# Kernel tuning notes

Measured on AMD Instinct MI355X. Metric: run time of the kernel, lower is better.

Reference implementation:

```python
import jax, jax.numpy as jnp
import numpy as np

N_NODES = 100000
N_EDGES = 1600000
D_IN = 64
D_OUT = 64


def setup_inputs() -> dict:
    key = jax.random.key(0)
    k1, k2, k3, k4, k5 = jax.random.split(key, 5)
    feat = jax.random.normal(k1, (N_NODES, D_IN), dtype=jnp.float32)
    src = jax.random.randint(k2, (N_EDGES,), 0, N_NODES, dtype=jnp.int64)
    dst = jax.random.randint(k3, (N_EDGES,), 0, N_NODES, dtype=jnp.int64)
    # Xavier-uniform init with relu gain, as in reset_parameters()
    gain = np.sqrt(2.0)
    bound = gain * np.sqrt(6.0 / (D_IN + D_OUT))
    W_self = jax.random.uniform(k4, (D_OUT, D_IN), minval=-bound, maxval=bound, dtype=jnp.float32)
    W_neigh = jax.random.uniform(k5, (D_OUT, D_IN), minval=-bound, maxval=bound, dtype=jnp.float32)
    return {"feat": feat, "src": src, "dst": dst, "W_self": W_self, "W_neigh": W_neigh}


def _spmm_mean(feat, src, dst, n_nodes):
    # Mean neighbor aggregation: for each dst node, average src features.
    gathered = feat[src]  # [E, D] irregular gather
    agg = jax.ops.segment_sum(gathered, dst, num_segments=n_nodes)  # [N, D]
    deg = jax.ops.segment_sum(jnp.ones((src.shape[0],), feat.dtype), dst, num_segments=n_nodes)
    return agg / jnp.maximum(deg, 1.0)[:, None]


def reference(feat, src, dst, W_self, W_neigh):
    neigh = _spmm_mean(feat, src, dst, feat.shape[0])  # [N, D_in]
    # rst = fc_self(feat) + fc_neigh(SpMM(feat))
    return feat @ W_self.T + neigh @ W_neigh.T
```

## Files before the change

kernel.cpp:

```cpp
#include <hip/hip_runtime.h>
#include <hip/hip_fp16.h>

#define N_NODES 100000
#define N_EDGES 1600000
#define D 64
#define ZROW 100000

#define NPB   240
#define NB    417
#define CAP   8192

#define EPB   8192
#define PBLK  ((N_EDGES + EPB - 1) / EPB)
#define CONVB 256

#define W3_FF16     0u
#define W3_PACKED   12800128u
#define W3_GCUR     (W3_PACKED + 4u * NB * CAP)
#define W3_NODEOFF  (W3_GCUR + 4u * NB)
#define W3_NODECNT  (W3_NODEOFF + 4u * N_NODES)
#define W3_W16      (W3_NODECNT + 4u * N_NODES)
#define W3_NEED     (W3_W16 + 16384u)

typedef __attribute__((ext_vector_type(8))) _Float16 half8;
typedef __attribute__((ext_vector_type(4))) float f32x4;

__device__ inline unsigned int h2bits(__half2 h) { return *(unsigned int*)&h; }
__device__ inline __half2 bits2h(unsigned int u) { return *(__half2*)&u; }
__device__ inline __half2 h2shfl_xor(__half2 x, int mask) {
    int i = *(int*)&x;
    i = __shfl_xor(i, mask);
    return *(__half2*)&i;
}

__global__ __launch_bounds__(1024) void k_part_conv(
    const float* __restrict__ feat,
    const int* __restrict__ src, const int* __restrict__ dst,
    const float* __restrict__ Ws, const float* __restrict__ Wn,
    unsigned int* __restrict__ ff16, unsigned int* __restrict__ w16,
    int* __restrict__ gcur, int* __restrict__ packed)
{
    __shared__ int recs[EPB];
    __shared__ int cnt[NB];
    __shared__ int scn[512];
    __shared__ int pos[NB];
    __shared__ int cur[NB];
    __shared__ int dlt[NB];

    const int bid = blockIdx.x;
    const int t   = threadIdx.x;

    if (bid >= PBLK) {
        if (bid < PBLK + CONVB) {
            const int total = N_NODES * D / 8;
            for (int i = (bid - PBLK) * 1024 + t; i < total; i += CONVB * 1024) {
                const float4 x = ((const float4*)feat)[i * 2];
                const float4 y = ((const float4*)feat)[i * 2 + 1];
                uint4 o;
                o.x = h2bits(__floats2half2_rn(x.x, x.y));
                o.y = h2bits(__floats2half2_rn(x.z, x.w));
                o.z = h2bits(__floats2half2_rn(y.x, y.y));
                o.w = h2bits(__floats2half2_rn(y.z, y.w));
                ((uint4*)ff16)[i] = o;
            }
        } else {
            for (int i = t; i < 2048; i += 1024) {
                w16[i]        = h2bits(__floats2half2_rn(Ws[2 * i], Ws[2 * i + 1]));
                w16[2048 + i] = h2bits(__floats2half2_rn(Wn[2 * i], Wn[2 * i + 1]));
            }
            if (t < 32) ff16[ZROW * 32 + t] = 0;
        }
        return;
    }

    const int e0 = bid * EPB;
    const int nE = min(EPB, N_EDGES - e0);

    for (int i = t; i < NB; i += 1024) cnt[i] = 0;
    __syncthreads();

    int pk[8], bk[8];
    #pragma unroll
    for (int k = 0; k < 8; ++k) {
        const int i = t + k * 1024;
        if (i < nE) {
            const int d  = dst[e0 + i];
            const int b  = d / NPB;
            const int dl = d - b * NPB;
            pk[k] = src[e0 + i] | (dl << 17);
            bk[k] = b;
            atomicAdd(&cnt[b], 1);
        } else {
            bk[k] = -1;
        }
    }
    __syncthreads();

    if (t < 512) scn[t] = (t < NB) ? cnt[t] : 0;
    __syncthreads();
    for (int o = 1; o < 512; o <<= 1) {
        int x = 0;
        if (t < 512 && t >= o) x = scn[t - o];
        __syncthreads();
        if (t < 512) scn[t] += x;
        __syncthreads();
    }
    if (t < NB) {
        const int v    = cnt[t];
        const int excl = scn[t] - v;
        pos[t] = excl;
        cur[t] = excl;
        dlt[t] = atomicAdd(&gcur[t], v);
    }
    __syncthreads();

    #pragma unroll
    for (int k = 0; k < 8; ++k) {
        if (bk[k] >= 0) {
            const int p = atomicAdd(&cur[bk[k]], 1);
            recs[p] = pk[k];
        }
    }
    __syncthreads();

    const int w    = t >> 6;
    const int lane = t & 63;
    for (int b = w; b < NB; b += 16) {
        const int n = cnt[b];
        const int o = pos[b];
        const int g = b * CAP + dlt[b];
        for (int i = lane; i < n; i += 64)
            packed[g + i] = recs[o + i];
    }
}

__global__ __launch_bounds__(512) void k_sortb(
    const int* __restrict__ gcur,
    int* packed,
    int* __restrict__ node_off, int* __restrict__ node_cnt)
{
    __shared__ int recs[CAP];
    __shared__ int lcnt[256];
    __shared__ int sc[256];
    __shared__ int lcur[NPB];

    const int t      = threadIdx.x;
    const int bucket = blockIdx.x;
    const int base   = bucket * CAP;
    int total = gcur[bucket];
    if (total > CAP) total = CAP;

    if (t < 256) lcnt[t] = 0;
    __syncthreads();

    for (int i = t; i < total; i += 512) {
        const int r = packed[base + i];
        recs[i] = r;
        atomicAdd(&lcnt[r >> 17], 1);
    }
    __syncthreads();

    if (t < 256) sc[t] = lcnt[t];
    __syncthreads();
    for (int o = 1; o < 256; o <<= 1) {
        int x = 0;
        if (t < 256 && t >= o) x = sc[t - o];
        __syncthreads();
        if (t < 256) sc[t] += x;
        __syncthreads();
    }

    if (t < NPB) {
        const int excl = sc[t] - lcnt[t];
        lcur[t] = excl;
        const int n = bucket * NPB + t;
        if (n < N_NODES) {
            node_off[n] = base + excl;
            node_cnt[n] = lcnt[t];
        }
    }
    __syncthreads();

    for (int i = t; i < total; i += 512) {
        const int r   = recs[i];
        const int pos = atomicAdd(&lcur[r >> 17], 1);
        packed[base + pos] = r & 0x1FFFF;
    }
}

__global__ __launch_bounds__(256) void k_agg_f16(
    const unsigned int* __restrict__ ff16,
    const int* __restrict__ node_off,
    const int* __restrict__ node_cnt,
    const int* __restrict__ packed,
    float* __restrict__ out)
{
    const int gtid = blockIdx.x * 256 + threadIdx.x;
    const int n    = gtid >> 6;
    const int lane = gtid & 63;
    if (n >= N_NODES) return;

    const int start = node_off[n];
    const int deg   = node_cnt[n];
    const int sub   = lane >> 3;
    const int chunk = lane & 7;

    __half2 a0 = __floats2half2_rn(0.f, 0.f);
    __half2 a1 = a0, a2 = a0, a3 = a0;

    for (int b = 0; b < deg; b += 64) {
        const int rem = min(deg - b, 64);
        int p = ZROW;
        if (lane < rem) p = packed[start + b + lane];

        const int npair = (rem + 15) >> 4;
        for (int q = 0; q < npair; ++q) {
            const int e0 = q * 16 + sub;
            const int s0 = __shfl(p, e0)     & 0x1FFFF;
            const int s1 = __shfl(p, e0 + 8) & 0x1FFFF;
            const uint4 v0 = ((const uint4*)ff16)[(size_t)s0 * 8 + chunk];
            const uint4 v1 = ((const uint4*)ff16)[(size_t)s1 * 8 + chunk];
            a0 += bits2h(v0.x);
            a1 += bits2h(v0.y);
            a2 += bits2h(v0.z);
            a3 += bits2h(v0.w);
            a0 += bits2h(v1.x);
            a1 += bits2h(v1.y);
            a2 += bits2h(v1.z);
            a3 += bits2h(v1.w);
        }
    }

    #pragma unroll
    for (int mask = 8; mask <= 32; mask <<= 1) {
        a0 += h2shfl_xor(a0, mask);
        a1 += h2shfl_xor(a1, mask);
        a2 += h2shfl_xor(a2, mask);
        a3 += h2shfl_xor(a3, mask);
    }

    if (lane < 8) {
        const float inv = 1.0f / (float)((deg > 0) ? deg : 1);
        uint4 mb;
        mb.x = h2bits(__floats2half2_rn(__low2float(a0) * inv, __high2float(a0) * inv));
        mb.y = h2bits(__floats2half2_rn(__low2float(a1) * inv, __high2float(a1) * inv));
        mb.z = h2bits(__floats2half2_rn(__low2float(a2) * inv, __high2float(a2) * inv));
        mb.w = h2bits(__floats2half2_rn(__low2float(a3) * inv, __high2float(a3) * inv));
        ((uint4*)out)[(size_t)n * 16 + lane] = mb;
    }
}

__global__ __launch_bounds__(256) void k_update_mfma(
    const unsigned int* __restrict__ ff16,
    const _Float16* __restrict__ w16,
    float* out)
{
    const int wv   = threadIdx.x >> 6;
    const int lane = threadIdx.x & 63;
    const int n0   = blockIdx.x * 64 + wv * 16;
    const int r16  = lane & 15;
    const int g    = lane >> 4;

    half8 bws[4][2], bwn[4][2];
    #pragma unroll
    for (int nt = 0; nt < 4; ++nt) {
        const int c = nt * 16 + r16;
        #pragma unroll
        for (int kt = 0; kt < 2; ++kt) {
            const int k0 = kt * 32 + g * 8;
            bws[nt][kt] = *(const half8*)(w16 + c * 64 + k0);
            bwn[nt][kt] = *(const half8*)(w16 + 4096 + c * 64 + k0);
        }
    }

    const int arow = n0 + r16;
    const int rc   = (arow < N_NODES) ? arow : (N_NODES - 1);

    f32x4 acc[4] = {{0.f,0.f,0.f,0.f}, {0.f,0.f,0.f,0.f},
                    {0.f,0.f,0.f,0.f}, {0.f,0.f,0.f,0.f}};

    #pragma unroll
    for (int kt = 0; kt < 2; ++kt) {
        const int k8 = kt * 4 + g;
        const uint4 af_u = ((const uint4*)ff16)[(size_t)rc * 8 + k8];
        const uint4 am_u = ((const uint4*)out )[(size_t)rc * 16 + k8];
        const half8 af = *(const half8*)&af_u;
        const half8 am = *(const half8*)&am_u;
        #pragma unroll
        for (int nt = 0; nt < 4; ++nt) {
            acc[nt] = __builtin_amdgcn_mfma_f32_16x16x32_f16(af, bws[nt][kt], acc[nt], 0, 0, 0);
            acc[nt] = __builtin_amdgcn_mfma_f32_16x16x32_f16(am, bwn[nt][kt], acc[nt], 0, 0, 0);
        }
    }

    #pragma unroll
    for (int nt = 0; nt < 4; ++nt) {
        #pragma unroll
        for (int r = 0; r < 4; ++r) {
            const int ro = n0 + g * 4 + r;
            if (ro < N_NODES)
                out[(size_t)ro * 64 + nt * 16 + r16] = acc[nt][r];
        }
    }
}

__global__ __launch_bounds__(256) void sage_scatter(
    const float* __restrict__ feat,
    const int*   __restrict__ src,
    const int*   __restrict__ dst,
    float*       __restrict__ agg,
    float*       __restrict__ deg)
{
    const int gtid = blockIdx.x * blockDim.x + threadIdx.x;
    const int edge = gtid >> 6;
    const int lane = gtid & 63;
    if (edge >= N_EDGES) return;
    const int s = src[edge];
    const int d = dst[edge];
    atomicAdd(&agg[d * D + lane], feat[s * D + lane]);
    if (lane == 0) atomicAdd(&deg[d], 1.0f);
}

#define RL(v, l) __int_as_float(__builtin_amdgcn_readlane(__float_as_int(v), (l)))

__global__ __launch_bounds__(256) void k_update_div(
    const float* __restrict__ feat,
    const float* __restrict__ Ws,
    const float* __restrict__ Wn,
    const float* __restrict__ deg,
    float* out)
{
    const int wid   = (blockIdx.x * 256 + threadIdx.x) >> 6;
    const int lane  = threadIdx.x & 63;
    const int nwave = (gridDim.x * 256) >> 6;

    const float4* Ws4 = (const float4*)Ws;
    const float4* Wn4 = (const float4*)Wn;
    float4 ws[16], wn[16];
    #pragma unroll
    for (int j = 0; j < 16; ++j) {
        ws[j] = Ws4[lane * 16 + j];
        wn[j] = Wn4[lane * 16 + j];
    }

    for (int n = wid; n < N_NODES; n += nwave) {
        const float f = feat[n * D + lane];
        const float a = out[n * D + lane] / fmaxf(deg[n], 1.0f);
        float s0 = 0.f, s1 = 0.f, m0 = 0.f, m1 = 0.f;
        #pragma unroll
        for (int j = 0; j < 16; ++j) {
            const float4 w_s = ws[j];
            const float4 w_n = wn[j];
            s0 = fmaf(RL(f, 4 * j + 0), w_s.x, s0);
            s1 = fmaf(RL(f, 4 * j + 1), w_s.y, s1);
            s0 = fmaf(RL(f, 4 * j + 2), w_s.z, s0);
            s1 = fmaf(RL(f, 4 * j + 3), w_s.w, s1);
            m0 = fmaf(RL(a, 4 * j + 0), w_n.x, m0);
            m1 = fmaf(RL(a, 4 * j + 1), w_n.y, m1);
            m0 = fmaf(RL(a, 4 * j + 2), w_n.z, m0);
            m1 = fmaf(RL(a, 4 * j + 3), w_n.w, m1);
        }
        out[n * D + lane] = (s0 + s1) + (m0 + m1);
    }
}

extern "C" void kernel_launch(void* const* d_in, const int* in_sizes, int n_in,
                              void* d_out, int out_size, void* d_ws, size_t ws_size,
                              hipStream_t stream) {
    const float* feat = (const float*)d_in[0];
    const int*   src  = (const int*)d_in[1];
    const int*   dst  = (const int*)d_in[2];
    const float* Ws   = (const float*)d_in[3];
    const float* Wn   = (const float*)d_in[4];
    float* out = (float*)d_out;
    char*  ws  = (char*)d_ws;

    if (ws_size >= W3_NEED) {
        unsigned int* ff16 = (unsigned int*)(ws + W3_FF16);
        int* packed = (int*)(ws + W3_PACKED);
        int* gcur   = (int*)(ws + W3_GCUR);
        int* noff   = (int*)(ws + W3_NODEOFF);
        int* ncnt   = (int*)(ws + W3_NODECNT);
        unsigned int* w16u = (unsigned int*)(ws + W3_W16);

        hipMemsetAsync(gcur, 0, (size_t)NB * sizeof(int), stream);

        k_part_conv  <<<PBLK + CONVB + 1, 1024, 0, stream>>>(
            feat, src, dst, Ws, Wn, ff16, w16u, gcur, packed);
        k_sortb      <<<NB, 512, 0, stream>>>(gcur, packed, noff, ncnt);
        k_agg_f16    <<<(N_NODES * 64 + 255) / 256, 256, 0, stream>>>(
            ff16, noff, ncnt, packed, out);
        k_update_mfma<<<(N_NODES + 63) / 64, 256, 0, stream>>>(
            ff16, (const _Float16*)w16u, out);
    } else {
        float* deg = (float*)ws;
        hipMemsetAsync(out, 0, (size_t)N_NODES * D * sizeof(float), stream);
        hipMemsetAsync(deg, 0, (size_t)N_NODES * sizeof(float), stream);
        sage_scatter<<<(N_EDGES * 64) / 256, 256, 0, stream>>>(feat, src, dst, out, deg);
        k_update_div<<<1024, 256, 0, stream>>>(feat, Ws, Wn, deg, out);
    }
}
```

Before: 98.19 us.

## Split fp16 features into column planes for cache-local gather aggregation

Converts the fp16 feature table into four column planes of 16 features each, transposed through LDS, and writes the neighbor means into a separate plane-laid-out buffer instead of reusing the output. The aggregation kernel now uses a block-to-plane mapping so each plane (about 3.2 MB) is more likely to stay resident in L2 during the random gather. Each wave now handles two nodes with 16 edge lanes each. This trades repeated index reads (four times) and an extra workspace buffer for better cache locality. The zero-row setup for ZROW was removed, and the padded plane rows rely on the conversion blocks writing zeros.

Result: slower. 118.1 us (+20.3%).

```diff
diff --git a/kernel.cpp b/kernel.cpp
--- a/kernel.cpp
+++ b/kernel.cpp
@@ -12,14 +12,18 @@
 
 #define EPB   8192
 #define PBLK  ((N_EDGES + EPB - 1) / EPB)
-#define CONVB 256
-
-#define W3_FF16     0u
-#define W3_PACKED   12800128u
+#define CONV2 782
+
+#define PSN   100352
+#define PSU   (PSN * 2)
+
+#define W3_FFP      0u
+#define W3_MEANP    12845056u
+#define W3_PACKED   25690112u
 #define W3_GCUR     (W3_PACKED + 4u * NB * CAP)
 #define W3_NODEOFF  (W3_GCUR + 4u * NB)
 #define W3_NODECNT  (W3_NODEOFF + 4u * N_NODES)
-#define W3_W16      (W3_NODECNT + 4u * N_NODES)
+#define W3_W16      ((W3_NODECNT + 4u * N_NODES + 15u) & ~15u)
 #define W3_NEED     (W3_W16 + 16384u)
 
 typedef __attribute__((ext_vector_type(8))) _Float16 half8;
@@ -37,7 +41,7 @@
     const float* __restrict__ feat,
     const int* __restrict__ src, const int* __restrict__ dst,
     const float* __restrict__ Ws, const float* __restrict__ Wn,
-    unsigned int* __restrict__ ff16, unsigned int* __restrict__ w16,
+    uint4* __restrict__ ffp, unsigned int* __restrict__ w16,
     int* __restrict__ gcur, int* __restrict__ packed)
 {
     __shared__ int recs[EPB];
@@ -51,24 +55,38 @@
     const int t   = threadIdx.x;
 
     if (bid >= PBLK) {
-        if (bid < PBLK + CONVB) {
-            const int total = N_NODES * D / 8;
-            for (int i = (bid - PBLK) * 1024 + t; i < total; i += CONVB * 1024) {
-                const float4 x = ((const float4*)feat)[i * 2];
-                const float4 y = ((const float4*)feat)[i * 2 + 1];
-                uint4 o;
-                o.x = h2bits(__floats2half2_rn(x.x, x.y));
-                o.y = h2bits(__floats2half2_rn(x.z, x.w));
-                o.z = h2bits(__floats2half2_rn(y.x, y.y));
-                o.w = h2bits(__floats2half2_rn(y.z, y.w));
-                ((uint4*)ff16)[i] = o;
+        if (bid < PBLK + CONV2) {
+            uint4* lds = (uint4*)recs;
+            const int n0 = (bid - PBLK) * 128;
+            {
+                const int j  = t >> 3;
+                const int c8 = t & 7;
+                const int n  = n0 + j;
+                uint4 u = make_uint4(0u, 0u, 0u, 0u);
+                if (n < N_NODES) {
+                    const float4 x = *(const float4*)(feat + (size_t)n * 64 + c8 * 8);
+                    const float4 y = *(const float4*)(feat + (size_t)n * 64 + c8 * 8 + 4);
+                    u.x = h2bits(__floats2half2_rn(x.x, x.y));
+                    u.y = h2bits(__floats2half2_rn(x.z, x.w));
+                    u.z = h2bits(__floats2half2_rn(y.x, y.y));
+                    u.w = h2bits(__floats2half2_rn(y.z, y.w));
+                }
+                lds[j * 9 + c8] = u;
+            }
+            __syncthreads();
+            {
+                const int p    = t >> 8;
+                const int rem  = t & 255;
+                const int jj   = rem >> 1;
+                const int half = rem & 1;
+                const int n    = n0 + jj;
+                ffp[(size_t)p * PSU + n * 2 + half] = lds[jj * 9 + (p * 2 + half)];
             }
         } else {
             for (int i = t; i < 2048; i += 1024) {
                 w16[i]        = h2bits(__floats2half2_rn(Ws[2 * i], Ws[2 * i + 1]));
                 w16[2048 + i] = h2bits(__floats2half2_rn(Wn[2 * i], Wn[2 * i + 1]));
             }
-            if (t < 32) ff16[ZROW * 32 + t] = 0;
         }
         return;
     }
@@ -188,72 +206,63 @@
     }
 }
 
-__global__ __launch_bounds__(256) void k_agg_f16(
-    const unsigned int* __restrict__ ff16,
+__global__ __launch_bounds__(256) void k_agg_plane(
+    const uint4* __restrict__ ffp,
     const int* __restrict__ node_off,
     const int* __restrict__ node_cnt,
     const int* __restrict__ packed,
-    float* __restrict__ out)
-{
-    const int gtid = blockIdx.x * 256 + threadIdx.x;
-    const int n    = gtid >> 6;
-    const int lane = gtid & 63;
-    if (n >= N_NODES) return;
+    uint4* __restrict__ meanp)
+{
+    const int bid  = blockIdx.x;
+    const int c    = bid & 3;
+    const int nb   = (bid >> 2) * 8;
+    const int t    = threadIdx.x;
+    const int wv   = t >> 6;
+    const int lane = t & 63;
+    const int half = lane & 1;
+    const int el   = (lane & 31) >> 1;
+    const int n    = nb + wv * 2 + (lane >> 5);
 
     const int start = node_off[n];
     const int deg   = node_cnt[n];
-    const int sub   = lane >> 3;
-    const int chunk = lane & 7;
+    const uint4* plane = ffp + (size_t)c * PSU;
 
     __half2 a0 = __floats2half2_rn(0.f, 0.f);
     __half2 a1 = a0, a2 = a0, a3 = a0;
 
-    for (int b = 0; b < deg; b += 64) {
-        const int rem = min(deg - b, 64);
-        int p = ZROW;
-        if (lane < rem) p = packed[start + b + lane];
-
-        const int npair = (rem + 15) >> 4;
-        for (int q = 0; q < npair; ++q) {
-            const int e0 = q * 16 + sub;
-            const int s0 = __shfl(p, e0)     & 0x1FFFF;
-            const int s1 = __shfl(p, e0 + 8) & 0x1FFFF;
-            const uint4 v0 = ((const uint4*)ff16)[(size_t)s0 * 8 + chunk];
-            const uint4 v1 = ((const uint4*)ff16)[(size_t)s1 * 8 + chunk];
-            a0 += bits2h(v0.x);
-            a1 += bits2h(v0.y);
-            a2 += bits2h(v0.z);
-            a3 += bits2h(v0.w);
-            a0 += bits2h(v1.x);
-            a1 += bits2h(v1.y);
-            a2 += bits2h(v1.z);
-            a3 += bits2h(v1.w);
-        }
-    }
-
-    #pragma unroll
-    for (int mask = 8; mask <= 32; mask <<= 1) {
+    for (int e = el; __any(e < deg); e += 16) {
+        const int p = (e < deg) ? packed[start + e] : ZROW;
+        const uint4 v = plane[p * 2 + half];
+        a0 += bits2h(v.x);
+        a1 += bits2h(v.y);
+        a2 += bits2h(v.z);
+        a3 += bits2h(v.w);
+    }
+
+    #pragma unroll
+    for (int mask = 2; mask <= 16; mask <<= 1) {
         a0 += h2shfl_xor(a0, mask);
         a1 += h2shfl_xor(a1, mask);
         a2 += h2shfl_xor(a2, mask);
         a3 += h2shfl_xor(a3, mask);
     }
 
-    if (lane < 8) {
-        const float inv = 1.0f / (float)((deg > 0) ? deg : 1);
+    if (el == 0) {
+        const float inv = 1.0f / (float)max(deg, 1);
         uint4 mb;
         mb.x = h2bits(__floats2half2_rn(__low2float(a0) * inv, __high2float(a0) * inv));
         mb.y = h2bits(__floats2half2_rn(__low2float(a1) * inv, __high2float(a1) * inv));
         mb.z = h2bits(__floats2half2_rn(__low2float(a2) * inv, __high2float(a2) * inv));
         mb.w = h2bits(__floats2half2_rn(__low2float(a3) * inv, __high2float(a3) * inv));
-        ((uint4*)out)[(size_t)n * 16 + lane] = mb;
+        meanp[(size_t)c * PSU + n * 2 + half] = mb;
     }
 }
 
 __global__ __launch_bounds__(256) void k_update_mfma(
-    const unsigned int* __restrict__ ff16,
+    const uint4* __restrict__ ffp,
+    const uint4* __restrict__ meanp,
     const _Float16* __restrict__ w16,
-    float* out)
+    float* __restrict__ out)
 {
     const int wv   = threadIdx.x >> 6;
     const int lane = threadIdx.x & 63;
@@ -264,12 +273,12 @@
     half8 bws[4][2], bwn[4][2];
     #pragma unroll
     for (int nt = 0; nt < 4; ++nt) {
-        const int c = nt * 16 + r16;
+        const int cc = nt * 16 + r16;
         #pragma unroll
         for (int kt = 0; kt < 2; ++kt) {
             const int k0 = kt * 32 + g * 8;
-            bws[nt][kt] = *(const half8*)(w16 + c * 64 + k0);
-            bwn[nt][kt] = *(const half8*)(w16 + 4096 + c * 64 + k0);
+            bws[nt][kt] = *(const half8*)(w16 + cc * 64 + k0);
+            bwn[nt][kt] = *(const half8*)(w16 + 4096 + cc * 64 + k0);
         }
     }
 
@@ -282,8 +291,9 @@
     #pragma unroll
     for (int kt = 0; kt < 2; ++kt) {
         const int k8 = kt * 4 + g;
-        const uint4 af_u = ((const uint4*)ff16)[(size_t)rc * 8 + k8];
-        const uint4 am_u = ((const uint4*)out )[(size_t)rc * 16 + k8];
+        const size_t idx = (size_t)(k8 >> 1) * PSU + (size_t)rc * 2 + (k8 & 1);
+        const uint4 af_u = ffp[idx];
+        const uint4 am_u = meanp[idx];
         const half8 af = *(const half8*)&af_u;
         const half8 am = *(const half8*)&am_u;
         #pragma unroll
@@ -376,22 +386,23 @@
     char*  ws  = (char*)d_ws;
 
     if (ws_size >= W3_NEED) {
-        unsigned int* ff16 = (unsigned int*)(ws + W3_FF16);
-        int* packed = (int*)(ws + W3_PACKED);
-        int* gcur   = (int*)(ws + W3_GCUR);
-        int* noff   = (int*)(ws + W3_NODEOFF);
-        int* ncnt   = (int*)(ws + W3_NODECNT);
+        uint4* ffp   = (uint4*)(ws + W3_FFP);
+        uint4* meanp = (uint4*)(ws + W3_MEANP);
+        int* packed  = (int*)(ws + W3_PACKED);
+        int* gcur    = (int*)(ws + W3_GCUR);
+        int* noff    = (int*)(ws + W3_NODEOFF);
+        int* ncnt    = (int*)(ws + W3_NODECNT);
         unsigned int* w16u = (unsigned int*)(ws + W3_W16);
 
         hipMemsetAsync(gcur, 0, (size_t)NB * sizeof(int), stream);
 
-        k_part_conv  <<<PBLK + CONVB + 1, 1024, 0, stream>>>(
-            feat, src, dst, Ws, Wn, ff16, w16u, gcur, packed);
+        k_part_conv  <<<PBLK + CONV2 + 1, 1024, 0, stream>>>(
+            feat, src, dst, Ws, Wn, ffp, w16u, gcur, packed);
         k_sortb      <<<NB, 512, 0, stream>>>(gcur, packed, noff, ncnt);
-        k_agg_f16    <<<(N_NODES * 64 + 255) / 256, 256, 0, stream>>>(
-            ff16, noff, ncnt, packed, out);
+        k_agg_plane  <<<(N_NODES / 8) * 4, 256, 0, stream>>>(
+            ffp, noff, ncnt, packed, meanp);
         k_update_mfma<<<(N_NODES + 63) / 64, 256, 0, stream>>>(
-            ff16, (const _Float16*)w16u, out);
+            ffp, meanp, (const _Float16*)w16u, out);
     } else {
         float* deg = (float*)ws;
         hipMemsetAsync(out, 0, (size_t)N_NODES * D * sizeof(float), stream);
```

## Move feature conversion into sort kernel and make aggregation persistent with prefetch

Applied to the files above, without the earlier changes.

The fp32-to-fp16 feature and weight conversion moves out of the partition kernel and into the per-bucket sort kernel, so the partition launch covers only edges and the conversion runs alongside the sort blocks. The aggregation kernel becomes a persistent grid-stride loop over a fixed number of waves, and each wave prefetches the next node's offset, degree and first neighbor indices while it aggregates the current node. This is meant to hide index-load latency and rebalance work across the stages. In exchange there are fewer waves in flight during aggregation and the sort kernel gets extra register and launch pressure.

Result: faster. 94.23 us (-4.0%).

```diff
diff --git a/kernel.cpp b/kernel.cpp
--- a/kernel.cpp
+++ b/kernel.cpp
@@ -12,7 +12,11 @@
 
 #define EPB   8192
 #define PBLK  ((N_EDGES + EPB - 1) / EPB)
-#define CONVB 256
+
+#define CONVB 782
+
+#define AGG_BLOCKS 2048
+#define NWAVES (AGG_BLOCKS * 4)
 
 #define W3_FF16     0u
 #define W3_PACKED   12800128u
@@ -33,11 +37,8 @@
     return *(__half2*)&i;
 }
 
-__global__ __launch_bounds__(1024) void k_part_conv(
-    const float* __restrict__ feat,
+__global__ __launch_bounds__(1024) void k_partition(
     const int* __restrict__ src, const int* __restrict__ dst,
-    const float* __restrict__ Ws, const float* __restrict__ Wn,
-    unsigned int* __restrict__ ff16, unsigned int* __restrict__ w16,
     int* __restrict__ gcur, int* __restrict__ packed)
 {
     __shared__ int recs[EPB];
@@ -49,32 +50,8 @@
 
     const int bid = blockIdx.x;
     const int t   = threadIdx.x;
-
-    if (bid >= PBLK) {
-        if (bid < PBLK + CONVB) {
-            const int total = N_NODES * D / 8;
-            for (int i = (bid - PBLK) * 1024 + t; i < total; i += CONVB * 1024) {
-                const float4 x = ((const float4*)feat)[i * 2];
-                const float4 y = ((const float4*)feat)[i * 2 + 1];
-                uint4 o;
-                o.x = h2bits(__floats2half2_rn(x.x, x.y));
-                o.y = h2bits(__floats2half2_rn(x.z, x.w));
-                o.z = h2bits(__floats2half2_rn(y.x, y.y));
-                o.w = h2bits(__floats2half2_rn(y.z, y.w));
-                ((uint4*)ff16)[i] = o;
-            }
-        } else {
-            for (int i = t; i < 2048; i += 1024) {
-                w16[i]        = h2bits(__floats2half2_rn(Ws[2 * i], Ws[2 * i + 1]));
-                w16[2048 + i] = h2bits(__floats2half2_rn(Wn[2 * i], Wn[2 * i + 1]));
-            }
-            if (t < 32) ff16[ZROW * 32 + t] = 0;
-        }
-        return;
-    }
-
-    const int e0 = bid * EPB;
-    const int nE = min(EPB, N_EDGES - e0);
+    const int e0  = bid * EPB;
+    const int nE  = min(EPB, N_EDGES - e0);
 
     for (int i = t; i < NB; i += 1024) cnt[i] = 0;
     __syncthreads();
@@ -134,7 +111,10 @@
     }
 }
 
-__global__ __launch_bounds__(512) void k_sortb(
+__global__ __launch_bounds__(512) void k_sortb_conv(
+    const float* __restrict__ feat,
+    const float* __restrict__ Ws, const float* __restrict__ Wn,
+    unsigned int* __restrict__ ff16, unsigned int* __restrict__ w16,
     const int* __restrict__ gcur,
     int* packed,
     int* __restrict__ node_off, int* __restrict__ node_cnt)
@@ -144,8 +124,33 @@
     __shared__ int sc[256];
     __shared__ int lcur[NPB];
 
-    const int t      = threadIdx.x;
-    const int bucket = blockIdx.x;
+    const int bid = blockIdx.x;
+    const int t   = threadIdx.x;
+
+    if (bid >= NB) {
+        if (bid < NB + CONVB) {
+            const int total = N_NODES * D / 8;
+            for (int i = (bid - NB) * 512 + t; i < total; i += CONVB * 512) {
+                const float4 x = ((const float4*)feat)[i * 2];
+                const float4 y = ((const float4*)feat)[i * 2 + 1];
+                uint4 o;
+                o.x = h2bits(__floats2half2_rn(x.x, x.y));
+                o.y = h2bits(__floats2half2_rn(x.z, x.w));
+                o.z = h2bits(__floats2half2_rn(y.x, y.y));
+                o.w = h2bits(__floats2half2_rn(y.z, y.w));
+                ((uint4*)ff16)[i] = o;
+            }
+        } else {
+            for (int i = t; i < 2048; i += 512) {
+                w16[i]        = h2bits(__floats2half2_rn(Ws[2 * i], Ws[2 * i + 1]));
+                w16[2048 + i] = h2bits(__floats2half2_rn(Wn[2 * i], Wn[2 * i + 1]));
+            }
+            if (t < 32) ff16[ZROW * 32 + t] = 0;
+        }
+        return;
+    }
+
+    const int bucket = bid;
     const int base   = bucket * CAP;
     int total = gcur[bucket];
     if (total > CAP) total = CAP;
@@ -188,6 +193,28 @@
     }
 }
 
+__device__ inline void agg_chunk(
+    __half2& a0, __half2& a1, __half2& a2, __half2& a3,
+    int p, int m, int sub, int chunk, const unsigned int* __restrict__ ff16)
+{
+    const int npair = (m + 15) >> 4;
+    for (int q = 0; q < npair; ++q) {
+        const int e0 = q * 16 + sub;
+        const int s0 = __shfl(p, e0)     & 0x1FFFF;
+        const int s1 = __shfl(p, e0 + 8) & 0x1FFFF;
+        const uint4 v0 = ((const uint4*)ff16)[(size_t)s0 * 8 + chunk];
+        const uint4 v1 = ((const uint4*)ff16)[(size_t)s1 * 8 + chunk];
+        a0 += bits2h(v0.x);
+        a1 += bits2h(v0.y);
+        a2 += bits2h(v0.z);
+        a3 += bits2h(v0.w);
+        a0 += bits2h(v1.x);
+        a1 += bits2h(v1.y);
+        a2 += bits2h(v1.z);
+        a3 += bits2h(v1.w);
+    }
+}
+
 __global__ __launch_bounds__(256) void k_agg_f16(
     const unsigned int* __restrict__ ff16,
     const int* __restrict__ node_off,
@@ -195,58 +222,55 @@
     const int* __restrict__ packed,
     float* __restrict__ out)
 {
-    const int gtid = blockIdx.x * 256 + threadIdx.x;
-    const int n    = gtid >> 6;
-    const int lane = gtid & 63;
-    if (n >= N_NODES) return;
-
-    const int start = node_off[n];
-    const int deg   = node_cnt[n];
+    const int wid   = blockIdx.x * 4 + (threadIdx.x >> 6);
+    const int lane  = threadIdx.x & 63;
     const int sub   = lane >> 3;
     const int chunk = lane & 7;
 
-    __half2 a0 = __floats2half2_rn(0.f, 0.f);
-    __half2 a1 = a0, a2 = a0, a3 = a0;
-
-    for (int b = 0; b < deg; b += 64) {
-        const int rem = min(deg - b, 64);
-        int p = ZROW;
-        if (lane < rem) p = packed[start + b + lane];
-
-        const int npair = (rem + 15) >> 4;
-        for (int q = 0; q < npair; ++q) {
-            const int e0 = q * 16 + sub;
-            const int s0 = __shfl(p, e0)     & 0x1FFFF;
-            const int s1 = __shfl(p, e0 + 8) & 0x1FFFF;
-            const uint4 v0 = ((const uint4*)ff16)[(size_t)s0 * 8 + chunk];
-            const uint4 v1 = ((const uint4*)ff16)[(size_t)s1 * 8 + chunk];
-            a0 += bits2h(v0.x);
-            a1 += bits2h(v0.y);
-            a2 += bits2h(v0.z);
-            a3 += bits2h(v0.w);
-            a0 += bits2h(v1.x);
-            a1 += bits2h(v1.y);
-            a2 += bits2h(v1.z);
-            a3 += bits2h(v1.w);
-        }
-    }
-
-    #pragma unroll
-    for (int mask = 8; mask <= 32; mask <<= 1) {
-        a0 += h2shfl_xor(a0, mask);
-        a1 += h2shfl_xor(a1, mask);
-        a2 += h2shfl_xor(a2, mask);
-        a3 += h2shfl_xor(a3, mask);
-    }
-
-    if (lane < 8) {
-        const float inv = 1.0f / (float)((deg > 0) ? deg : 1);
-        uint4 mb;
-        mb.x = h2bits(__floats2half2_rn(__low2float(a0) * inv, __high2float(a0) * inv));
-        mb.y = h2bits(__floats2half2_rn(__low2float(a1) * inv, __high2float(a1) * inv));
-        mb.z = h2bits(__floats2half2_rn(__low2float(a2) * inv, __high2float(a2) * inv));
-        mb.w = h2bits(__floats2half2_rn(__low2float(a3) * inv, __high2float(a3) * inv));
-        ((uint4*)out)[(size_t)n * 16 + lane] = mb;
+    int n     = wid;
+    int start = node_off[n];
+    int deg   = node_cnt[n];
+    int p     = (lane < min(deg, 64)) ? packed[start + lane] : ZROW;
+
+    while (true) {
+        const int n1 = n + NWAVES;
+        int start1 = 0, deg1 = 0, p1 = ZROW;
+        if (n1 < N_NODES) {
+            start1 = node_off[n1];
+            deg1   = node_cnt[n1];
+            if (lane < min(deg1, 64)) p1 = packed[start1 + lane];
+        }
+
+        __half2 a0 = __floats2half2_rn(0.f, 0.f);
+        __half2 a1 = a0, a2 = a0, a3 = a0;
+
+        agg_chunk(a0, a1, a2, a3, p, min(deg, 64), sub, chunk, ff16);
+        for (int b = 64; b < deg; b += 64) {
+            const int rem = min(deg - b, 64);
+            const int pp  = (lane < rem) ? packed[start + b + lane] : ZROW;
+            agg_chunk(a0, a1, a2, a3, pp, rem, sub, chunk, ff16);
+        }
+
+        #pragma unroll
+        for (int mask = 8; mask <= 32; mask <<= 1) {
+            a0 += h2shfl_xor(a0, mask);
+            a1 += h2shfl_xor(a1, mask);
+            a2 += h2shfl_xor(a2, mask);
+            a3 += h2shfl_xor(a3, mask);
+        }
+
+        if (lane < 8) {
+            const float inv = 1.0f / (float)((deg > 0) ? deg : 1);
+            uint4 mb;
+            mb.x = h2bits(__floats2half2_rn(__low2float(a0) * inv, __high2float(a0) * inv));
+            mb.y = h2bits(__floats2half2_rn(__low2float(a1) * inv, __high2float(a1) * inv));
+            mb.z = h2bits(__floats2half2_rn(__low2float(a2) * inv, __high2float(a2) * inv));
+            mb.w = h2bits(__floats2half2_rn(__low2float(a3) * inv, __high2float(a3) * inv));
+            ((uint4*)out)[(size_t)n * 16 + lane] = mb;
+        }
+
+        if (n1 >= N_NODES) break;
+        n = n1; start = start1; deg = deg1; p = p1;
     }
 }
 
@@ -385,10 +409,10 @@
 
         hipMemsetAsync(gcur, 0, (size_t)NB * sizeof(int), stream);
 
-        k_part_conv  <<<PBLK + CONVB + 1, 1024, 0, stream>>>(
-            feat, src, dst, Ws, Wn, ff16, w16u, gcur, packed);
-        k_sortb      <<<NB, 512, 0, stream>>>(gcur, packed, noff, ncnt);
-        k_agg_f16    <<<(N_NODES * 64 + 255) / 256, 256, 0, stream>>>(
+        k_partition  <<<PBLK, 1024, 0, stream>>>(src, dst, gcur, packed);
+        k_sortb_conv <<<NB + CONVB + 1, 512, 0, stream>>>(
+            feat, Ws, Wn, ff16, w16u, gcur, packed, noff, ncnt);
+        k_agg_f16    <<<AGG_BLOCKS, 256, 0, stream>>>(
             ff16, noff, ncnt, packed, out);
         k_update_mfma<<<(N_NODES + 63) / 64, 256, 0, stream>>>(
             ff16, (const _Float16*)w16u, out);
```
